# Optimization experiments

Measured on AMD Instinct MI355X. Metric: run time of the kernel, lower is better.

Reference implementation:

```python
import jax, jax.numpy as jnp
import numpy as np
from jax import lax

B, T = 64, 2048
D_LSTM, D_ENC, D_ATT, N_F, K = 1024, 512, 128, 32, 31
PAD = (K - 1) // 2  # 15, 'same' padding as Tacotron2 LocationLayer


def setup_inputs() -> dict:
    key = jax.random.key(0)
    ks = jax.random.split(key, 11)
    def w(k, shape, fan_in):
        return jax.random.normal(k, shape, dtype=jnp.float32) / np.sqrt(fan_in)
    return {
        "query": jax.random.normal(ks[0], (B, 1, D_LSTM), dtype=jnp.float32),
        "memory": jax.random.normal(ks[1], (B, T, D_ENC), dtype=jnp.float32),
        "attention_weights_cat": jax.random.uniform(ks[2], (B, 2, T), dtype=jnp.float32),
        "Wq": w(ks[3], (D_ATT, D_LSTM), D_LSTM),
        "bq": jnp.zeros((D_ATT,), jnp.float32),
        "Wm": w(ks[4], (D_ATT, D_ENC), D_ENC),
        "bm": jnp.zeros((D_ATT,), jnp.float32),
        "Wconv": w(ks[5], (N_F, 2, K), 2 * K),  # Conv1d weight [out, in, k], bias=False
        "Wloc": w(ks[6], (D_ATT, N_F), N_F),     # location dense, bias=False
        "Wv": w(ks[7], (1, D_ATT), D_ATT),
        "bv": jnp.zeros((1,), jnp.float32),
    }


def reference(query, memory, attention_weights_cat, Wq, bq, Wm, bm, Wconv, Wloc, Wv, bv):
    # query_layer: [B,1,D_LSTM] -> [B,1,D_ATT]
    q = query @ Wq.T + bq
    # memory_layer: [B,T,D_ENC] -> [B,T,D_ATT]
    k = memory @ Wm.T + bm
    # location_layer: Conv1d same-pad over time, then dense to D_ATT
    conv = lax.conv_general_dilated(
        attention_weights_cat, Wconv, window_strides=(1,),
        padding=[(PAD, PAD)], dimension_numbers=("NCH", "OIH", "NCH"))  # [B,N_F,T]
    loc = jnp.einsum("bft,af->bta", conv, Wloc)  # [B,T,D_ATT]
    # energies: v^T tanh(q + k + loc) -> [B,T]
    energies = (jnp.tanh(q + k + loc) @ Wv.T + bv).squeeze(-1)
    attention_weights = jax.nn.softmax(energies, axis=1)  # [B,T]
    attention_context = jnp.einsum("bt,btd->bd", attention_weights, memory)  # [B,D_ENC]
    return attention_context, attention_weights
```

## Files before the change

kernel.cpp:

```cpp
#include <hip/hip_runtime.h>
#include <math.h>

#define B_ 64
#define T_ 2048
#define DL 1024
#define DE 512
#define DA 128
#define NF 32
#define KW 31
#define PADW 15
#define TT 128
#define LDA 40

typedef short bf16x8 __attribute__((ext_vector_type(8)));
typedef float f32x4 __attribute__((ext_vector_type(4)));

__device__ __forceinline__ void split_bf16(float x, unsigned short &hi, unsigned short &lo) {
    unsigned u = __float_as_uint(x);
    unsigned short h = (unsigned short)((u + 0x7FFFu + ((u >> 16) & 1u)) >> 16);
    float hf = __uint_as_float((unsigned)h << 16);
    float l = x - hf;
    unsigned ul = __float_as_uint(l);
    hi = h;
    lo = (unsigned short)((ul + 0x7FFFu + ((ul >> 16) & 1u)) >> 16);
}

__device__ __forceinline__ float fast_tanh(float x) {
    x = fminf(fmaxf(x, -15.f), 15.f);
    float e2 = __expf(2.f * x);
    return (e2 - 1.f) * __builtin_amdgcn_rcpf(e2 + 1.f);
}

__global__ __launch_bounds__(256) void prep_kernel(const float* __restrict__ Wm,
                                                   unsigned short* __restrict__ bg_hi,
                                                   unsigned short* __restrict__ bg_lo) {
    int i = blockIdx.x * 256 + threadIdx.x;
    unsigned short h, l;
    split_bf16(Wm[i], h, l);
    bg_hi[i] = h;
    bg_lo[i] = l;
}

__global__ __launch_bounds__(128) void q_kernel(const float* __restrict__ query,
                                                const float* __restrict__ Wq,
                                                const float* __restrict__ bq,
                                                float* __restrict__ qbuf) {
    int b = blockIdx.x;
    int a = threadIdx.x;
    __shared__ __align__(16) float qs[DL];
    for (int i = threadIdx.x; i < DL; i += 128) qs[i] = query[(size_t)b * DL + i];
    __syncthreads();
    const float* wrow = Wq + (size_t)a * DL;
    float acc = 0.f;
#pragma unroll 8
    for (int i = 0; i < DL; i += 4) {
        float4 w = *(const float4*)(wrow + i);
        float4 q4 = *(const float4*)(qs + i);
        acc += w.x * q4.x + w.y * q4.y + w.z * q4.z + w.w * q4.w;
    }
    qbuf[(size_t)b * DA + a] = acc + bq[a];
}

__global__ __launch_bounds__(256, 3) void energy_kernel(
    const float* __restrict__ mem,
    const float* __restrict__ attw,
    const unsigned short* __restrict__ bg_hi,
    const unsigned short* __restrict__ bg_lo,
    const float* __restrict__ bm,
    const float* __restrict__ Wconv,
    const float* __restrict__ Wloc,
    const float* __restrict__ Wv,
    const float* __restrict__ bv,
    const float* __restrict__ qbuf,
    float* __restrict__ e_out)
{
    __shared__ __align__(16) unsigned short Ahi[TT * LDA];
    __shared__ __align__(16) unsigned short Alo[TT * LDA];
    __shared__ __align__(16) unsigned short Bhi[DA * LDA];
    __shared__ __align__(16) unsigned short Blo[DA * LDA];
    __shared__ __align__(16) float attw_s[2 * 160];
    __shared__ __align__(16) float wconv_s[NF * 64];
    __shared__ float qb_s[DA], wv_s[DA];
    __shared__ float e_part[2][TT];

    const int tid = threadIdx.x;
    const int b = blockIdx.y;
    const int t0 = blockIdx.x * TT;
    const int lane = tid & 63;
    const int wave = tid >> 6;
    const int wm = wave & 1, wn = wave >> 1;
    const int m = lane & 15;
    const int q8 = (lane >> 4) * 8;

    if (tid < DA) {
        qb_s[tid] = qbuf[(size_t)b * DA + tid] + bm[tid];
        wv_s[tid] = Wv[tid];
    }

    for (int i = tid; i < 2 * (TT + KW - 1); i += 256) {
        int c = i / 158, j = i % 158;
        int t = t0 - PADW + j;
        attw_s[c * 160 + j] = (t >= 0 && t < T_) ? attw[((size_t)b * 2 + c) * T_ + t] : 0.f;
    }
    for (int i = tid; i < NF * 2 * KW; i += 256) {
        int f = i / 62, r = i % 62;
        wconv_s[f * 64 + r] = Wconv[i];
    }
    __syncthreads();

    for (int i = tid; i < TT * NF; i += 256) {
        int t = i >> 5, f = i & 31;
        const float* w0 = wconv_s + f * 64;
        const float* a0 = attw_s + t;
        const float* a1 = attw_s + 160 + t;
        float s = 0.f;
#pragma unroll
        for (int k = 0; k < KW; ++k) s += w0[k] * a0[k] + w0[31 + k] * a1[k];
        unsigned short h, l;
        split_bf16(s, h, l);
        Ahi[t * LDA + f] = h;
        Alo[t * LDA + f] = l;
    }
    for (int i = tid; i < DA * NF; i += 256) {
        int a = i >> 5, f = i & 31;
        unsigned short h, l;
        split_bf16(Wloc[a * NF + f], h, l);
        Bhi[a * LDA + f] = h;
        Blo[a * LDA + f] = l;
    }
    __syncthreads();

    f32x4 acc[4][4];
#pragma unroll
    for (int mi = 0; mi < 4; ++mi)
#pragma unroll
        for (int ni = 0; ni < 4; ++ni) {
            f32x4 z = {0.f, 0.f, 0.f, 0.f};
            acc[mi][ni] = z;
        }

    auto mfma_step = [&]() {
        bf16x8 ah[4], al[4];
#pragma unroll
        for (int mi = 0; mi < 4; ++mi) {
            int r = (wm * 64 + mi * 16 + m) * LDA + q8;
            ah[mi] = *(const bf16x8*)(Ahi + r);
            al[mi] = *(const bf16x8*)(Alo + r);
        }
#pragma unroll
        for (int ni = 0; ni < 4; ++ni) {
            int r = (wn * 64 + ni * 16 + m) * LDA + q8;
            bf16x8 bh = *(const bf16x8*)(Bhi + r);
            bf16x8 bl = *(const bf16x8*)(Blo + r);
#pragma unroll
            for (int mi = 0; mi < 4; ++mi) {
                acc[mi][ni] = __builtin_amdgcn_mfma_f32_16x16x32_bf16(ah[mi], bh, acc[mi][ni], 0, 0, 0);
                acc[mi][ni] = __builtin_amdgcn_mfma_f32_16x16x32_bf16(ah[mi], bl, acc[mi][ni], 0, 0, 0);
                acc[mi][ni] = __builtin_amdgcn_mfma_f32_16x16x32_bf16(al[mi], bh, acc[mi][ni], 0, 0, 0);
            }
        }
    };

    mfma_step();

    const size_t mem_base = ((size_t)b * T_ + t0) * DE;
    for (int c = 0; c < 16; ++c) {
        const int k0 = c * 32;
        __syncthreads();
#pragma unroll
        for (int r = 0; r < 4; ++r) {
            int idx = tid + 256 * r;
            int t = idx >> 3, c4 = (idx & 7) * 4;
            float4 v = *(const float4*)(mem + mem_base + (size_t)t * DE + k0 + c4);
            unsigned short h0, l0, h1, l1, h2, l2, h3, l3;
            split_bf16(v.x, h0, l0);
            split_bf16(v.y, h1, l1);
            split_bf16(v.z, h2, l2);
            split_bf16(v.w, h3, l3);
            ushort4 hv = {h0, h1, h2, h3};
            ushort4 lv = {l0, l1, l2, l3};
            *(ushort4*)(Ahi + t * LDA + c4) = hv;
            *(ushort4*)(Alo + t * LDA + c4) = lv;
        }
#pragma unroll
        for (int r = 0; r < 2; ++r) {
            int idx = tid + 256 * r;
            int a = idx >> 2, c8 = (idx & 3) * 8;
            *(uint4*)(Bhi + a * LDA + c8) = *(const uint4*)(bg_hi + (size_t)a * DE + k0 + c8);
            *(uint4*)(Blo + a * LDA + c8) = *(const uint4*)(bg_lo + (size_t)a * DE + k0 + c8);
        }
        __syncthreads();
        mfma_step();
    }

    float wvr[4], qbr[4];
#pragma unroll
    for (int ni = 0; ni < 4; ++ni) {
        int a = wn * 64 + ni * 16 + m;
        wvr[ni] = wv_s[a];
        qbr[ni] = qb_s[a];
    }
    float bvv = bv[0];
#pragma unroll
    for (int mi = 0; mi < 4; ++mi) {
#pragma unroll
        for (int reg = 0; reg < 4; ++reg) {
            float s = 0.f;
#pragma unroll
            for (int ni = 0; ni < 4; ++ni)
                s += wvr[ni] * fast_tanh(acc[mi][ni][reg] + qbr[ni]);
            s += __shfl_xor(s, 1, 64);
            s += __shfl_xor(s, 2, 64);
            s += __shfl_xor(s, 4, 64);
            s += __shfl_xor(s, 8, 64);
            if (m == 0)
                e_part[wn][wm * 64 + mi * 16 + (lane >> 4) * 4 + reg] = s;
        }
    }
    __syncthreads();
    if (tid < TT)
        e_out[(size_t)b * T_ + t0 + tid] = e_part[0][tid] + e_part[1][tid] + bvv;
}

__global__ __launch_bounds__(256) void softmax_kernel(const float* __restrict__ e,
                                                      float* __restrict__ wout) {
    int b = blockIdx.x;
    int tid = threadIdx.x;
    __shared__ float red[4];
    float v[8];
    float m = -1e30f;
#pragma unroll
    for (int r = 0; r < 8; ++r) {
        v[r] = e[(size_t)b * T_ + r * 256 + tid];
        m = fmaxf(m, v[r]);
    }
#pragma unroll
    for (int off = 1; off < 64; off <<= 1) m = fmaxf(m, __shfl_xor(m, off, 64));
    if ((tid & 63) == 0) red[tid >> 6] = m;
    __syncthreads();
    m = fmaxf(fmaxf(red[0], red[1]), fmaxf(red[2], red[3]));
    __syncthreads();
    float s = 0.f;
#pragma unroll
    for (int r = 0; r < 8; ++r) {
        v[r] = expf(v[r] - m);
        s += v[r];
    }
#pragma unroll
    for (int off = 1; off < 64; off <<= 1) s += __shfl_xor(s, off, 64);
    if ((tid & 63) == 0) red[tid >> 6] = s;
    __syncthreads();
    s = red[0] + red[1] + red[2] + red[3];
    float inv = 1.0f / s;
#pragma unroll
    for (int r = 0; r < 8; ++r) wout[(size_t)b * T_ + r * 256 + tid] = v[r] * inv;
}

__global__ __launch_bounds__(256) void ctx_partial_kernel(const float* __restrict__ mem,
                                                          const float* __restrict__ w,
                                                          float* __restrict__ partial) {
    int b = blockIdx.y, tc = blockIdx.x;
    int tid = threadIdx.x;
    __shared__ float ws_s[128];
    __shared__ float red[512];
    if (tid < 128) ws_s[tid] = w[(size_t)b * T_ + tc * 128 + tid];
    __syncthreads();
    int d = (tid & 127) * 4;
    int th = tid >> 7;
    const float* mp = mem + ((size_t)b * T_ + tc * 128 + th * 64) * DE + d;
    float a0 = 0.f, a1 = 0.f, a2 = 0.f, a3 = 0.f;
#pragma unroll 8
    for (int t = 0; t < 64; ++t) {
        float4 v = *(const float4*)(mp + (size_t)t * DE);
        float wv = ws_s[th * 64 + t];
        a0 += wv * v.x; a1 += wv * v.y; a2 += wv * v.z; a3 += wv * v.w;
    }
    if (th == 1) {
        float* r = red + (tid & 127) * 4;
        r[0] = a0; r[1] = a1; r[2] = a2; r[3] = a3;
    }
    __syncthreads();
    if (th == 0) {
        const float* r = red + tid * 4;
        float* pp = partial + ((size_t)b * 16 + tc) * DE + d;
        pp[0] = a0 + r[0]; pp[1] = a1 + r[1]; pp[2] = a2 + r[2]; pp[3] = a3 + r[3];
    }
}

__global__ __launch_bounds__(512) void ctx_reduce_kernel(const float* __restrict__ partial,
                                                         float* __restrict__ ctx) {
    int b = blockIdx.x;
    int d = threadIdx.x;
    float s = 0.f;
#pragma unroll
    for (int j = 0; j < 16; ++j) s += partial[((size_t)b * 16 + j) * DE + d];
    ctx[(size_t)b * DE + d] = s;
}

extern "C" void kernel_launch(void* const* d_in, const int* in_sizes, int n_in,
                              void* d_out, int out_size, void* d_ws, size_t ws_size,
                              hipStream_t stream) {
    const float* query  = (const float*)d_in[0];
    const float* memory = (const float*)d_in[1];
    const float* attw   = (const float*)d_in[2];
    const float* Wq     = (const float*)d_in[3];
    const float* bq     = (const float*)d_in[4];
    const float* Wm     = (const float*)d_in[5];
    const float* bm     = (const float*)d_in[6];
    const float* Wconv  = (const float*)d_in[7];
    const float* Wloc   = (const float*)d_in[8];
    const float* Wv     = (const float*)d_in[9];
    const float* bv     = (const float*)d_in[10];

    float* out = (float*)d_out;
    float* ctx_out = out;
    float* w_out = out + B_ * DE;

    float* ws = (float*)d_ws;
    float* qbuf = ws;
    float* ebuf = qbuf + B_ * DA;
    float* partial = ebuf + (size_t)B_ * T_;
    unsigned short* bg_hi = (unsigned short*)(partial + (size_t)B_ * 16 * DE);
    unsigned short* bg_lo = bg_hi + DA * DE;

    prep_kernel<<<dim3(DA * DE / 256), dim3(256), 0, stream>>>(Wm, bg_hi, bg_lo);
    q_kernel<<<dim3(B_), dim3(128), 0, stream>>>(query, Wq, bq, qbuf);
    energy_kernel<<<dim3(T_ / TT, B_), dim3(256), 0, stream>>>(
        memory, attw, bg_hi, bg_lo, bm, Wconv, Wloc, Wv, bv, qbuf, ebuf);
    softmax_kernel<<<dim3(B_), dim3(256), 0, stream>>>(ebuf, w_out);
    ctx_partial_kernel<<<dim3(16, B_), dim3(256), 0, stream>>>(memory, w_out, partial);
    ctx_reduce_kernel<<<dim3(B_), dim3(512), 0, stream>>>(partial, ctx_out);
}
```

Before: 541.8 us.

## Double-buffer memory tiles via direct global-to-LDS loads and split bf16 in registers

The energy kernel now streams fp32 memory tiles straight into a double-buffered, XOR-swizzled LDS buffer using global_load_lds, prefetching the next K-chunk while MFMAs run on the current one. The hi/lo bf16 split of memory moves from the staging store to register time after the LDS read. Wm fragments are loaded directly from global into registers instead of through LDS. Wloc splitting moves into the prep kernel. This removes one barrier per chunk and the register round-trip for staging, but relies on hand-written waitcnt/barrier asm and repeats the split work for each wave that reads a row.

```diff
diff --git a/kernel.cpp b/kernel.cpp
--- a/kernel.cpp
+++ b/kernel.cpp
@@ -10,7 +10,6 @@
 #define KW 31
 #define PADW 15
 #define TT 128
-#define LDA 40
 
 typedef short bf16x8 __attribute__((ext_vector_type(8)));
 typedef float f32x4 __attribute__((ext_vector_type(4)));
@@ -25,20 +24,47 @@
     lo = (unsigned short)((ul + 0x7FFFu + ((ul >> 16) & 1u)) >> 16);
 }
 
+__device__ __forceinline__ void split8(const float4 &v0, const float4 &v1, bf16x8 &hi, bf16x8 &lo) {
+    unsigned short h, l;
+    split_bf16(v0.x, h, l); hi[0] = (short)h; lo[0] = (short)l;
+    split_bf16(v0.y, h, l); hi[1] = (short)h; lo[1] = (short)l;
+    split_bf16(v0.z, h, l); hi[2] = (short)h; lo[2] = (short)l;
+    split_bf16(v0.w, h, l); hi[3] = (short)h; lo[3] = (short)l;
+    split_bf16(v1.x, h, l); hi[4] = (short)h; lo[4] = (short)l;
+    split_bf16(v1.y, h, l); hi[5] = (short)h; lo[5] = (short)l;
+    split_bf16(v1.z, h, l); hi[6] = (short)h; lo[6] = (short)l;
+    split_bf16(v1.w, h, l); hi[7] = (short)h; lo[7] = (short)l;
+}
+
 __device__ __forceinline__ float fast_tanh(float x) {
     x = fminf(fmaxf(x, -15.f), 15.f);
     float e2 = __expf(2.f * x);
     return (e2 - 1.f) * __builtin_amdgcn_rcpf(e2 + 1.f);
 }
 
+__device__ __forceinline__ void gload_lds16(const float* g, float* l) {
+    __builtin_amdgcn_global_load_lds((const __attribute__((address_space(1))) void*)g,
+                                     (__attribute__((address_space(3))) void*)l, 16, 0, 0);
+}
+
 __global__ __launch_bounds__(256) void prep_kernel(const float* __restrict__ Wm,
+                                                   const float* __restrict__ Wloc,
                                                    unsigned short* __restrict__ bg_hi,
-                                                   unsigned short* __restrict__ bg_lo) {
+                                                   unsigned short* __restrict__ bg_lo,
+                                                   unsigned short* __restrict__ bw_hi,
+                                                   unsigned short* __restrict__ bw_lo) {
     int i = blockIdx.x * 256 + threadIdx.x;
     unsigned short h, l;
-    split_bf16(Wm[i], h, l);
-    bg_hi[i] = h;
-    bg_lo[i] = l;
+    if (i < DA * DE) {
+        split_bf16(Wm[i], h, l);
+        bg_hi[i] = h;
+        bg_lo[i] = l;
+    } else {
+        int j = i - DA * DE;
+        split_bf16(Wloc[j], h, l);
+        bw_hi[j] = h;
+        bw_lo[j] = l;
+    }
 }
 
 __global__ __launch_bounds__(128) void q_kernel(const float* __restrict__ query,
@@ -66,18 +92,16 @@
     const float* __restrict__ attw,
     const unsigned short* __restrict__ bg_hi,
     const unsigned short* __restrict__ bg_lo,
+    const unsigned short* __restrict__ bw_hi,
+    const unsigned short* __restrict__ bw_lo,
     const float* __restrict__ bm,
     const float* __restrict__ Wconv,
-    const float* __restrict__ Wloc,
     const float* __restrict__ Wv,
     const float* __restrict__ bv,
     const float* __restrict__ qbuf,
     float* __restrict__ e_out)
 {
-    __shared__ __align__(16) unsigned short Ahi[TT * LDA];
-    __shared__ __align__(16) unsigned short Alo[TT * LDA];
-    __shared__ __align__(16) unsigned short Bhi[DA * LDA];
-    __shared__ __align__(16) unsigned short Blo[DA * LDA];
+    __shared__ __align__(16) float Ast[2][TT * NF];
     __shared__ __align__(16) float attw_s[2 * 160];
     __shared__ __align__(16) float wconv_s[NF * 64];
     __shared__ float qb_s[DA], wv_s[DA];
@@ -90,7 +114,9 @@
     const int wave = tid >> 6;
     const int wm = wave & 1, wn = wave >> 1;
     const int m = lane & 15;
-    const int q8 = (lane >> 4) * 8;
+    const int g = lane >> 4;
+    const int q8 = g * 8;
+    const int s0 = g * 2;
 
     if (tid < DA) {
         qb_s[tid] = qbuf[(size_t)b * DA + tid] + bm[tid];
@@ -116,19 +142,28 @@
         float s = 0.f;
 #pragma unroll
         for (int k = 0; k < KW; ++k) s += w0[k] * a0[k] + w0[31 + k] * a1[k];
-        unsigned short h, l;
-        split_bf16(s, h, l);
-        Ahi[t * LDA + f] = h;
-        Alo[t * LDA + f] = l;
-    }
-    for (int i = tid; i < DA * NF; i += 256) {
-        int a = i >> 5, f = i & 31;
-        unsigned short h, l;
-        split_bf16(Wloc[a * NF + f], h, l);
-        Bhi[a * LDA + f] = h;
-        Blo[a * LDA + f] = l;
-    }
-    __syncthreads();
+        Ast[0][t * 32 + (((f >> 2) ^ (t & 7)) << 2) + (f & 3)] = s;
+    }
+
+    const size_t mem_base = ((size_t)b * T_ + t0) * DE;
+
+#pragma unroll
+    for (int r = 0; r < 4; ++r) {
+        int idx = tid + 256 * r;
+        int t = idx >> 3, sp = idx & 7;
+        gload_lds16(mem + mem_base + (size_t)t * DE + ((sp ^ (t & 7)) << 2),
+                    &Ast[1][idx << 2]);
+    }
+
+    bf16x8 bh[4], bl[4];
+#pragma unroll
+    for (int ni = 0; ni < 4; ++ni) {
+        int a = wn * 64 + ni * 16 + m;
+        bh[ni] = *(const bf16x8*)(bw_hi + a * NF + q8);
+        bl[ni] = *(const bf16x8*)(bw_lo + a * NF + q8);
+    }
+
+    asm volatile("s_waitcnt lgkmcnt(0)\n\ts_barrier" ::: "memory");
 
     f32x4 acc[4][4];
 #pragma unroll
@@ -139,60 +174,56 @@
             acc[mi][ni] = z;
         }
 
-    auto mfma_step = [&]() {
+    auto compute = [&](const float* buf) {
         bf16x8 ah[4], al[4];
 #pragma unroll
         for (int mi = 0; mi < 4; ++mi) {
-            int r = (wm * 64 + mi * 16 + m) * LDA + q8;
-            ah[mi] = *(const bf16x8*)(Ahi + r);
-            al[mi] = *(const bf16x8*)(Alo + r);
-        }
-#pragma unroll
-        for (int ni = 0; ni < 4; ++ni) {
-            int r = (wn * 64 + ni * 16 + m) * LDA + q8;
-            bf16x8 bh = *(const bf16x8*)(Bhi + r);
-            bf16x8 bl = *(const bf16x8*)(Blo + r);
+            int t = wm * 64 + mi * 16 + m;
+            int tx = t & 7;
+            const float* rowp = buf + t * 32;
+            float4 v0 = *(const float4*)(rowp + ((s0 ^ tx) << 2));
+            float4 v1 = *(const float4*)(rowp + (((s0 + 1) ^ tx) << 2));
+            split8(v0, v1, ah[mi], al[mi]);
+        }
+        __builtin_amdgcn_s_setprio(1);
+#pragma unroll
+        for (int ni = 0; ni < 4; ++ni)
 #pragma unroll
             for (int mi = 0; mi < 4; ++mi) {
-                acc[mi][ni] = __builtin_amdgcn_mfma_f32_16x16x32_bf16(ah[mi], bh, acc[mi][ni], 0, 0, 0);
-                acc[mi][ni] = __builtin_amdgcn_mfma_f32_16x16x32_bf16(ah[mi], bl, acc[mi][ni], 0, 0, 0);
-                acc[mi][ni] = __builtin_amdgcn_mfma_f32_16x16x32_bf16(al[mi], bh, acc[mi][ni], 0, 0, 0);
+                acc[mi][ni] = __builtin_amdgcn_mfma_f32_16x16x32_bf16(ah[mi], bh[ni], acc[mi][ni], 0, 0, 0);
+                acc[mi][ni] = __builtin_amdgcn_mfma_f32_16x16x32_bf16(ah[mi], bl[ni], acc[mi][ni], 0, 0, 0);
+                acc[mi][ni] = __builtin_amdgcn_mfma_f32_16x16x32_bf16(al[mi], bh[ni], acc[mi][ni], 0, 0, 0);
             }
-        }
+        __builtin_amdgcn_s_setprio(0);
     };
 
-    mfma_step();
-
-    const size_t mem_base = ((size_t)b * T_ + t0) * DE;
+    compute(&Ast[0][0]);
+
+#pragma unroll 1
     for (int c = 0; c < 16; ++c) {
         const int k0 = c * 32;
-        __syncthreads();
-#pragma unroll
-        for (int r = 0; r < 4; ++r) {
-            int idx = tid + 256 * r;
-            int t = idx >> 3, c4 = (idx & 7) * 4;
-            float4 v = *(const float4*)(mem + mem_base + (size_t)t * DE + k0 + c4);
-            unsigned short h0, l0, h1, l1, h2, l2, h3, l3;
-            split_bf16(v.x, h0, l0);
-            split_bf16(v.y, h1, l1);
-            split_bf16(v.z, h2, l2);
-            split_bf16(v.w, h3, l3);
-            ushort4 hv = {h0, h1, h2, h3};
-            ushort4 lv = {l0, l1, l2, l3};
-            *(ushort4*)(Ahi + t * LDA + c4) = hv;
-            *(ushort4*)(Alo + t * LDA + c4) = lv;
-        }
-#pragma unroll
-        for (int r = 0; r < 2; ++r) {
-            int idx = tid + 256 * r;
-            int a = idx >> 2, c8 = (idx & 3) * 8;
-            *(uint4*)(Bhi + a * LDA + c8) = *(const uint4*)(bg_hi + (size_t)a * DE + k0 + c8);
-            *(uint4*)(Blo + a * LDA + c8) = *(const uint4*)(bg_lo + (size_t)a * DE + k0 + c8);
-        }
-        __syncthreads();
-        mfma_step();
-    }
-
+#pragma unroll
+        for (int ni = 0; ni < 4; ++ni) {
+            int a = wn * 64 + ni * 16 + m;
+            bh[ni] = *(const bf16x8*)(bg_hi + (size_t)a * DE + k0 + q8);
+            bl[ni] = *(const bf16x8*)(bg_lo + (size_t)a * DE + k0 + q8);
+        }
+        asm volatile("s_waitcnt vmcnt(4)\n\ts_barrier" ::: "memory");
+        {
+            const int k0n = ((c + 1) & 15) * 32;
+            const float* gk = mem + mem_base + k0n;
+            float* lb = &Ast[c & 1][0];
+#pragma unroll
+            for (int r = 0; r < 4; ++r) {
+                int idx = tid + 256 * r;
+                int t = idx >> 3, sp = idx & 7;
+                gload_lds16(gk + (size_t)t * DE + ((sp ^ (t & 7)) << 2), lb + (idx << 2));
+            }
+        }
+        compute(&Ast[(c + 1) & 1][0]);
+    }
+
+    __syncthreads();
     float wvr[4], qbr[4];
 #pragma unroll
     for (int ni = 0; ni < 4; ++ni) {
@@ -322,11 +353,14 @@
     float* partial = ebuf + (size_t)B_ * T_;
     unsigned short* bg_hi = (unsigned short*)(partial + (size_t)B_ * 16 * DE);
     unsigned short* bg_lo = bg_hi + DA * DE;
-
-    prep_kernel<<<dim3(DA * DE / 256), dim3(256), 0, stream>>>(Wm, bg_hi, bg_lo);
+    unsigned short* bw_hi = bg_lo + DA * DE;
+    unsigned short* bw_lo = bw_hi + DA * NF;
+
+    prep_kernel<<<dim3((DA * DE + DA * NF) / 256), dim3(256), 0, stream>>>(
+        Wm, Wloc, bg_hi, bg_lo, bw_hi, bw_lo);
     q_kernel<<<dim3(B_), dim3(128), 0, stream>>>(query, Wq, bq, qbuf);
     energy_kernel<<<dim3(T_ / TT, B_), dim3(256), 0, stream>>>(
-        memory, attw, bg_hi, bg_lo, bm, Wconv, Wloc, Wv, bv, qbuf, ebuf);
+        memory, attw, bg_hi, bg_lo, bw_hi, bw_lo, bm, Wconv, Wv, bv, qbuf, ebuf);
     softmax_kernel<<<dim3(B_), dim3(256), 0, stream>>>(ebuf, w_out);
     ctx_partial_kernel<<<dim3(16, B_), dim3(256), 0, stream>>>(memory, w_out, partial);
     ctx_reduce_kernel<<<dim3(B_), dim3(512), 0, stream>>>(partial, ctx_out);
```

Measured after the change: 574.4 us. +6.0%, slower.

## Prefetch memory tiles into registers and regroup MFMAs in energy kernel

Applied to the files above, without the earlier changes.

The energy kernel now loads the next memory K-chunk into registers while the current chunk's MFMAs run, replacing the load-then-compute sequence with a software-pipelined register prefetch. It also uses raw s_barrier with an lgkmcnt wait, groups MFMAs by hi/lo pass under raised wave priority, and moves the Wloc bf16 split into the prep kernel. The extra prefetch registers lower occupancy from three to two blocks per CU, which may reduce latency hiding elsewhere.

```diff
diff --git a/kernel.cpp b/kernel.cpp
--- a/kernel.cpp
+++ b/kernel.cpp
@@ -32,13 +32,23 @@
 }
 
 __global__ __launch_bounds__(256) void prep_kernel(const float* __restrict__ Wm,
+                                                   const float* __restrict__ Wloc,
                                                    unsigned short* __restrict__ bg_hi,
-                                                   unsigned short* __restrict__ bg_lo) {
+                                                   unsigned short* __restrict__ bg_lo,
+                                                   unsigned short* __restrict__ bw_hi,
+                                                   unsigned short* __restrict__ bw_lo) {
     int i = blockIdx.x * 256 + threadIdx.x;
     unsigned short h, l;
-    split_bf16(Wm[i], h, l);
-    bg_hi[i] = h;
-    bg_lo[i] = l;
+    if (i < DA * DE) {
+        split_bf16(Wm[i], h, l);
+        bg_hi[i] = h;
+        bg_lo[i] = l;
+    } else {
+        int j = i - DA * DE;
+        split_bf16(Wloc[j], h, l);
+        bw_hi[j] = h;
+        bw_lo[j] = l;
+    }
 }
 
 __global__ __launch_bounds__(128) void q_kernel(const float* __restrict__ query,
@@ -61,14 +71,15 @@
     qbuf[(size_t)b * DA + a] = acc + bq[a];
 }
 
-__global__ __launch_bounds__(256, 3) void energy_kernel(
+__global__ __launch_bounds__(256, 2) void energy_kernel(
     const float* __restrict__ mem,
     const float* __restrict__ attw,
     const unsigned short* __restrict__ bg_hi,
     const unsigned short* __restrict__ bg_lo,
+    const unsigned short* __restrict__ bw_hi,
+    const unsigned short* __restrict__ bw_lo,
     const float* __restrict__ bm,
     const float* __restrict__ Wconv,
-    const float* __restrict__ Wloc,
     const float* __restrict__ Wv,
     const float* __restrict__ bv,
     const float* __restrict__ qbuf,
@@ -121,12 +132,12 @@
         Ahi[t * LDA + f] = h;
         Alo[t * LDA + f] = l;
     }
-    for (int i = tid; i < DA * NF; i += 256) {
-        int a = i >> 5, f = i & 31;
-        unsigned short h, l;
-        split_bf16(Wloc[a * NF + f], h, l);
-        Bhi[a * LDA + f] = h;
-        Blo[a * LDA + f] = l;
+#pragma unroll
+    for (int r = 0; r < 2; ++r) {
+        int idx = tid + 256 * r;
+        int a = idx >> 2, c8 = (idx & 3) * 8;
+        *(uint4*)(Bhi + a * LDA + c8) = *(const uint4*)(bw_hi + a * NF + c8);
+        *(uint4*)(Blo + a * LDA + c8) = *(const uint4*)(bw_lo + a * NF + c8);
     }
     __syncthreads();
 
@@ -140,7 +151,7 @@
         }
 
     auto mfma_step = [&]() {
-        bf16x8 ah[4], al[4];
+        bf16x8 ah[4], al[4], bh[4], bl[4];
 #pragma unroll
         for (int mi = 0; mi < 4; ++mi) {
             int r = (wm * 64 + mi * 16 + m) * LDA + q8;
@@ -150,33 +161,61 @@
 #pragma unroll
         for (int ni = 0; ni < 4; ++ni) {
             int r = (wn * 64 + ni * 16 + m) * LDA + q8;
-            bf16x8 bh = *(const bf16x8*)(Bhi + r);
-            bf16x8 bl = *(const bf16x8*)(Blo + r);
-#pragma unroll
-            for (int mi = 0; mi < 4; ++mi) {
-                acc[mi][ni] = __builtin_amdgcn_mfma_f32_16x16x32_bf16(ah[mi], bh, acc[mi][ni], 0, 0, 0);
-                acc[mi][ni] = __builtin_amdgcn_mfma_f32_16x16x32_bf16(ah[mi], bl, acc[mi][ni], 0, 0, 0);
-                acc[mi][ni] = __builtin_amdgcn_mfma_f32_16x16x32_bf16(al[mi], bh, acc[mi][ni], 0, 0, 0);
-            }
-        }
+            bh[ni] = *(const bf16x8*)(Bhi + r);
+            bl[ni] = *(const bf16x8*)(Blo + r);
+        }
+        __builtin_amdgcn_s_setprio(1);
+#pragma unroll
+        for (int ni = 0; ni < 4; ++ni)
+#pragma unroll
+            for (int mi = 0; mi < 4; ++mi)
+                acc[mi][ni] = __builtin_amdgcn_mfma_f32_16x16x32_bf16(ah[mi], bh[ni], acc[mi][ni], 0, 0, 0);
+#pragma unroll
+        for (int ni = 0; ni < 4; ++ni)
+#pragma unroll
+            for (int mi = 0; mi < 4; ++mi)
+                acc[mi][ni] = __builtin_amdgcn_mfma_f32_16x16x32_bf16(ah[mi], bl[ni], acc[mi][ni], 0, 0, 0);
+#pragma unroll
+        for (int ni = 0; ni < 4; ++ni)
+#pragma unroll
+            for (int mi = 0; mi < 4; ++mi)
+                acc[mi][ni] = __builtin_amdgcn_mfma_f32_16x16x32_bf16(al[mi], bh[ni], acc[mi][ni], 0, 0, 0);
+        __builtin_amdgcn_s_setprio(0);
     };
 
+    const size_t mem_base = ((size_t)b * T_ + t0) * DE;
+
+    float4 rA[4];
+#pragma unroll
+    for (int r = 0; r < 4; ++r) {
+        int idx = tid + 256 * r;
+        int t = idx >> 3, c4 = (idx & 7) * 4;
+        rA[r] = *(const float4*)(mem + mem_base + (size_t)t * DE + c4);
+    }
+
     mfma_step();
 
-    const size_t mem_base = ((size_t)b * T_ + t0) * DE;
+#pragma unroll 1
     for (int c = 0; c < 16; ++c) {
         const int k0 = c * 32;
-        __syncthreads();
+        asm volatile("s_barrier" ::: "memory");
+        uint4 rbh[2], rbl[2];
+#pragma unroll
+        for (int r = 0; r < 2; ++r) {
+            int idx = tid + 256 * r;
+            int a = idx >> 2, c8 = (idx & 3) * 8;
+            rbh[r] = *(const uint4*)(bg_hi + (size_t)a * DE + k0 + c8);
+            rbl[r] = *(const uint4*)(bg_lo + (size_t)a * DE + k0 + c8);
+        }
 #pragma unroll
         for (int r = 0; r < 4; ++r) {
             int idx = tid + 256 * r;
             int t = idx >> 3, c4 = (idx & 7) * 4;
-            float4 v = *(const float4*)(mem + mem_base + (size_t)t * DE + k0 + c4);
             unsigned short h0, l0, h1, l1, h2, l2, h3, l3;
-            split_bf16(v.x, h0, l0);
-            split_bf16(v.y, h1, l1);
-            split_bf16(v.z, h2, l2);
-            split_bf16(v.w, h3, l3);
+            split_bf16(rA[r].x, h0, l0);
+            split_bf16(rA[r].y, h1, l1);
+            split_bf16(rA[r].z, h2, l2);
+            split_bf16(rA[r].w, h3, l3);
             ushort4 hv = {h0, h1, h2, h3};
             ushort4 lv = {l0, l1, l2, l3};
             *(ushort4*)(Ahi + t * LDA + c4) = hv;
@@ -186,10 +225,19 @@
         for (int r = 0; r < 2; ++r) {
             int idx = tid + 256 * r;
             int a = idx >> 2, c8 = (idx & 3) * 8;
-            *(uint4*)(Bhi + a * LDA + c8) = *(const uint4*)(bg_hi + (size_t)a * DE + k0 + c8);
-            *(uint4*)(Blo + a * LDA + c8) = *(const uint4*)(bg_lo + (size_t)a * DE + k0 + c8);
-        }
-        __syncthreads();
+            *(uint4*)(Bhi + a * LDA + c8) = rbh[r];
+            *(uint4*)(Blo + a * LDA + c8) = rbl[r];
+        }
+        if (c < 15) {
+            const int k0n = k0 + 32;
+#pragma unroll
+            for (int r = 0; r < 4; ++r) {
+                int idx = tid + 256 * r;
+                int t = idx >> 3, c4 = (idx & 7) * 4;
+                rA[r] = *(const float4*)(mem + mem_base + (size_t)t * DE + k0n + c4);
+            }
+        }
+        asm volatile("s_waitcnt lgkmcnt(0)\n\ts_barrier" ::: "memory");
         mfma_step();
     }
 
@@ -322,11 +370,14 @@
     float* partial = ebuf + (size_t)B_ * T_;
     unsigned short* bg_hi = (unsigned short*)(partial + (size_t)B_ * 16 * DE);
     unsigned short* bg_lo = bg_hi + DA * DE;
-
-    prep_kernel<<<dim3(DA * DE / 256), dim3(256), 0, stream>>>(Wm, bg_hi, bg_lo);
+    unsigned short* bw_hi = bg_lo + DA * DE;
+    unsigned short* bw_lo = bw_hi + DA * NF;
+
+    prep_kernel<<<dim3((DA * DE + DA * NF) / 256), dim3(256), 0, stream>>>(
+        Wm, Wloc, bg_hi, bg_lo, bw_hi, bw_lo);
     q_kernel<<<dim3(B_), dim3(128), 0, stream>>>(query, Wq, bq, qbuf);
     energy_kernel<<<dim3(T_ / TT, B_), dim3(256), 0, stream>>>(
-        memory, attw, bg_hi, bg_lo, bm, Wconv, Wloc, Wv, bv, qbuf, ebuf);
+        memory, attw, bg_hi, bg_lo, bw_hi, bw_lo, bm, Wconv, Wv, bv, qbuf, ebuf);
     softmax_kernel<<<dim3(B_), dim3(256), 0, stream>>>(ebuf, w_out);
     ctx_partial_kernel<<<dim3(16, B_), dim3(256), 0, stream>>>(memory, w_out, partial);
     ctx_reduce_kernel<<<dim3(B_), dim3(512), 0, stream>>>(partial, ctx_out);
```

Measured after the change: 513.4 us. 5.2% less time.
